# Kernel tuning notes

Hardware: AMD Instinct MI355X
Metric: run time of the kernel (lower is better)

## Reference

```python
import jax, jax.numpy as jnp
import numpy as np

B, N_STATES, STATE_SIZE = 32768, 16, 32
ENC, HID, OUT = 64, 128, 8


def setup_inputs() -> dict:
    key = jax.random.key(0)
    ks = jax.random.split(key, 8)
    states = jax.random.normal(ks[0], (B, N_STATES, STATE_SIZE), dtype=jnp.float32)
    # validity flags: first element of each per-field state. agent state (index 0)
    # always valid; neighbor states valid with prob 0.7 (contiguity enforced in reference
    # via cumprod, matching the original while-loop semantics).
    flags = (jax.random.uniform(ks[1], (B, N_STATES)) < 0.7).astype(jnp.float32)
    flags = flags.at[:, 0].set(1.0)
    states = states.at[:, :, 0].set(flags)
    obs_flat = states.reshape(B, N_STATES * STATE_SIZE)
    s = 0.05
    return {
        "obs_flat": obs_flat,
        "W_enc": jax.random.normal(ks[2], (STATE_SIZE, ENC), dtype=jnp.float32) * s,
        "b_enc": jnp.zeros((ENC,), dtype=jnp.float32),
        "W_f": jax.random.normal(ks[3], (2 * ENC, HID), dtype=jnp.float32) * s,
        "b_f": jnp.zeros((HID,), dtype=jnp.float32),
        "W_dec": jax.random.normal(ks[4], (HID, OUT), dtype=jnp.float32) * s,
        "b_dec": jnp.zeros((OUT,), dtype=jnp.float32),
    }


def reference(obs_flat, W_enc, b_enc, W_f, b_f, W_dec, b_dec):
    Bsz = obs_flat.shape[0]
    states = obs_flat.reshape(Bsz, N_STATES, STATE_SIZE)          # [B,N,S]
    flags = states[:, :, 0]                                        # [B,N]
    # original: while-loop stops at first invalid state -> contiguous-prefix validity
    neigh_valid = jnp.cumprod((flags[:, 1:] == 1.0).astype(jnp.float32), axis=1)  # [B,N-1]
    enc = jax.nn.relu(jnp.einsum('bns,se->bne', states, W_enc) + b_enc)            # [B,N,E]
    agent_enc = enc[:, 0]                                          # [B,E]
    neigh_enc = enc[:, 1:]                                         # [B,N-1,E]
    cnt = jnp.sum(neigh_valid, axis=1)                             # [B]
    # mean aggregation over valid neighbors; zero vector if none (original aggregates [zeros])
    agg = jnp.einsum('bne,bn->be', neigh_enc, neigh_valid) / jnp.maximum(cnt, 1.0)[:, None]
    f_in = jnp.concatenate([agent_enc, agg], axis=-1)              # [B,2E]
    hidden = jax.nn.relu(f_in @ W_f + b_f)                         # [B,H]
    logits = hidden @ W_dec + b_dec                                # [B,O]
    return logits
```

## Files before the change

kernel.cpp:

```cpp
#include <hip/hip_runtime.h>
#include <stdint.h>

#define NB    32768
#define NS    16
#define SS    32
#define ENCD  64
#define HIDD  128
#define OUTD  8
#define BT    32
#define THREADS 256

typedef short bf16x8 __attribute__((ext_vector_type(8)));
typedef float f32x4  __attribute__((ext_vector_type(4)));

#define MFMA(a, b, c) __builtin_amdgcn_mfma_f32_16x16x32_bf16((a), (b), (c), 0, 0, 0)

__device__ __forceinline__ short bf16_bits(float x) {
  union { float f; uint32_t u; } v; v.f = x;
  uint32_t u = v.u;
  uint32_t r = (u + 0x7FFFu + ((u >> 16) & 1u)) >> 16;
  return (short)r;
}
__device__ __forceinline__ float bf16_to_f(short h) {
  union { uint32_t u; float f; } v;
  v.u = ((uint32_t)(uint16_t)h) << 16;
  return v.f;
}
__device__ __forceinline__ void split8(const float* f, bf16x8& hi, bf16x8& lo) {
#pragma unroll
  for (int j = 0; j < 8; ++j) {
    short h = bf16_bits(f[j]);
    hi[j] = h;
    lo[j] = bf16_bits(f[j] - bf16_to_f(h));
  }
}

__global__ __launch_bounds__(THREADS)
void gnn_fused(const float* __restrict__ obs,
               const float* __restrict__ W_enc,
               const float* __restrict__ b_enc,
               const float* __restrict__ W_f,
               const float* __restrict__ b_f,
               const float* __restrict__ W_dec,
               const float* __restrict__ b_dec,
               float* __restrict__ out)
{
  __shared__ __align__(16) float f_in[BT][132];
  __shared__ __align__(16) float hidn[BT][132];

  const int tid  = threadIdx.x;
  const int w    = tid >> 6;
  const int l    = tid & 63;
  const int m15  = l & 15;
  const int quad = l >> 4;
  const int b0   = blockIdx.x * BT;

  bf16x8 we_hi[4], we_lo[4];
  float  benc[4];
#pragma unroll
  for (int nt = 0; nt < 4; ++nt) {
    float f[8];
#pragma unroll
    for (int j = 0; j < 8; ++j)
      f[j] = W_enc[(size_t)(quad * 8 + j) * ENCD + nt * 16 + m15];
    split8(f, we_hi[nt], we_lo[nt]);
    benc[nt] = b_enc[nt * 16 + m15];
  }

  const float* bp = obs + (size_t)(b0 + w * 8) * (NS * SS) + m15 * SS + quad * 8;
  float4 c0 = ((const float4*)bp)[0];
  float4 c1 = ((const float4*)bp)[1];
#pragma unroll
  for (int i = 0; i < 8; ++i) {
    float4 n0, n1;
    if (i < 7) {
      const float* np = bp + (size_t)(i + 1) * (NS * SS);
      n0 = ((const float4*)np)[0];
      n1 = ((const float4*)np)[1];
    } else { n0 = c0; n1 = c1; }

    float f[8] = {c0.x, c0.y, c0.z, c0.w, c1.x, c1.y, c1.z, c1.w};

    unsigned long long bal = __ballot((l < 16) && (f[0] == 1.0f));
    int run = __builtin_ctzll(~(bal >> 1));
    float inv = 1.0f / fmaxf((float)run, 1.0f);

    bf16x8 ahi, alo;
    split8(f, ahi, alo);

    const int bi = w * 8 + i;
#pragma unroll
    for (int nt = 0; nt < 4; ++nt) {
      f32x4 acc = {0.f, 0.f, 0.f, 0.f};
      acc = MFMA(ahi, we_hi[nt], acc);
      acc = MFMA(alo, we_hi[nt], acc);
      acc = MFMA(ahi, we_lo[nt], acc);
      float s = 0.f, e0 = 0.f;
#pragma unroll
      for (int r = 0; r < 4; ++r) {
        int n = quad * 4 + r;
        float v = fmaxf(acc[r] + benc[nt], 0.f);
        if (n == 0) e0 = v;
        if (n >= 1 && n <= run) s += v;
      }
      s += __shfl_xor(s, 16, 64);
      s += __shfl_xor(s, 32, 64);
      if (quad == 0) {
        f_in[bi][nt * 16 + m15]      = e0;
        f_in[bi][64 + nt * 16 + m15] = s * inv;
      }
    }
    c0 = n0; c1 = n1;
  }
  __syncthreads();

  {
    const int mt = w >> 1;
    const int hb = (w & 1) * 4;

    bf16x8 fa_hi[4], fa_lo[4];
#pragma unroll
    for (int ks = 0; ks < 4; ++ks) {
      const float4* p = (const float4*)&f_in[mt * 16 + m15][ks * 32 + quad * 8];
      float4 a = p[0], b = p[1];
      float f[8] = {a.x, a.y, a.z, a.w, b.x, b.y, b.z, b.w};
      split8(f, fa_hi[ks], fa_lo[ks]);
    }

#pragma unroll
    for (int t = 0; t < 4; ++t) {
      const int h0 = (hb + t) * 16 + m15;
      f32x4 acc = {0.f, 0.f, 0.f, 0.f};
#pragma unroll
      for (int ks = 0; ks < 4; ++ks) {
        float f[8];
#pragma unroll
        for (int j = 0; j < 8; ++j)
          f[j] = W_f[(size_t)(ks * 32 + quad * 8 + j) * HIDD + h0];
        bf16x8 bhi, blo;
        split8(f, bhi, blo);
        acc = MFMA(fa_hi[ks], bhi, acc);
        acc = MFMA(fa_lo[ks], bhi, acc);
        acc = MFMA(fa_hi[ks], blo, acc);
      }
      const float bfv = b_f[h0];
#pragma unroll
      for (int r = 0; r < 4; ++r)
        hidn[mt * 16 + quad * 4 + r][h0] = fmaxf(acc[r] + bfv, 0.f);
    }
  }
  __syncthreads();

  if (w < 2) {
    bf16x8 ga_hi[4], ga_lo[4];
#pragma unroll
    for (int ks = 0; ks < 4; ++ks) {
      const float4* p = (const float4*)&hidn[w * 16 + m15][ks * 32 + quad * 8];
      float4 a = p[0], b = p[1];
      float f[8] = {a.x, a.y, a.z, a.w, b.x, b.y, b.z, b.w};
      split8(f, ga_hi[ks], ga_lo[ks]);
    }
    f32x4 acc = {0.f, 0.f, 0.f, 0.f};
#pragma unroll
    for (int ks = 0; ks < 4; ++ks) {
      float f[8];
#pragma unroll
      for (int j = 0; j < 8; ++j) {
        int k = ks * 32 + quad * 8 + j;
        f[j] = (m15 < OUTD) ? W_dec[(size_t)k * OUTD + m15] : 0.f;
      }
      bf16x8 bhi, blo;
      split8(f, bhi, blo);
      acc = MFMA(ga_hi[ks], bhi, acc);
      acc = MFMA(ga_lo[ks], bhi, acc);
      acc = MFMA(ga_hi[ks], blo, acc);
    }
    if (m15 < OUTD) {
      const float bd = b_dec[m15];
#pragma unroll
      for (int r = 0; r < 4; ++r) {
        const int m = w * 16 + quad * 4 + r;
        out[(size_t)(b0 + m) * OUTD + m15] = acc[r] + bd;
      }
    }
  }
}

extern "C" void kernel_launch(void* const* d_in, const int* in_sizes, int n_in,
                              void* d_out, int out_size, void* d_ws, size_t ws_size,
                              hipStream_t stream) {
  (void)in_sizes; (void)n_in; (void)d_ws; (void)ws_size; (void)out_size;
  const float* obs   = (const float*)d_in[0];
  const float* W_enc = (const float*)d_in[1];
  const float* b_enc = (const float*)d_in[2];
  const float* W_f   = (const float*)d_in[3];
  const float* b_f   = (const float*)d_in[4];
  const float* W_dec = (const float*)d_in[5];
  const float* b_dec = (const float*)d_in[6];
  float* out = (float*)d_out;

  dim3 grid(NB / BT);
  dim3 block(THREADS);
  gnn_fused<<<grid, block, 0, stream>>>(obs, W_enc, b_enc, W_f, b_f, W_dec, b_dec, out);
}
```

Baseline: 121.5 us.

## Switch split-precision MFMA from bf16 to fp16 and halve batch tile per block

```diff
diff --git a/kernel.cpp b/kernel.cpp
--- a/kernel.cpp
+++ b/kernel.cpp
@@ -7,35 +7,28 @@
 #define ENCD  64
 #define HIDD  128
 #define OUTD  8
-#define BT    32
+#define BT    16
 #define THREADS 256
 
-typedef short bf16x8 __attribute__((ext_vector_type(8)));
-typedef float f32x4  __attribute__((ext_vector_type(4)));
+typedef _Float16 half8  __attribute__((ext_vector_type(8)));
+typedef __fp16   fp16x2 __attribute__((ext_vector_type(2)));
+typedef float    f32x4  __attribute__((ext_vector_type(4)));
 
-#define MFMA(a, b, c) __builtin_amdgcn_mfma_f32_16x16x32_bf16((a), (b), (c), 0, 0, 0)
+#define MFMA(a, b, c) __builtin_amdgcn_mfma_f32_16x16x32_f16((a), (b), (c), 0, 0, 0)
 
-__device__ __forceinline__ short bf16_bits(float x) {
-  union { float f; uint32_t u; } v; v.f = x;
-  uint32_t u = v.u;
-  uint32_t r = (u + 0x7FFFu + ((u >> 16) & 1u)) >> 16;
-  return (short)r;
-}
-__device__ __forceinline__ float bf16_to_f(short h) {
-  union { uint32_t u; float f; } v;
-  v.u = ((uint32_t)(uint16_t)h) << 16;
-  return v.f;
-}
-__device__ __forceinline__ void split8(const float* f, bf16x8& hi, bf16x8& lo) {
+__device__ __forceinline__ void split8(const float* f, half8& hi, half8& lo) {
 #pragma unroll
-  for (int j = 0; j < 8; ++j) {
-    short h = bf16_bits(f[j]);
-    hi[j] = h;
-    lo[j] = bf16_bits(f[j] - bf16_to_f(h));
+  for (int j = 0; j < 8; j += 2) {
+    fp16x2 h  = __builtin_amdgcn_cvt_pkrtz(f[j], f[j + 1]);
+    float  r0 = f[j]     - (float)h[0];
+    float  r1 = f[j + 1] - (float)h[1];
+    fp16x2 l2 = __builtin_amdgcn_cvt_pkrtz(r0, r1);
+    hi[j] = (_Float16)(float)h[0];  hi[j + 1] = (_Float16)(float)h[1];
+    lo[j] = (_Float16)(float)l2[0]; lo[j + 1] = (_Float16)(float)l2[1];
   }
 }
 
-__global__ __launch_bounds__(THREADS)
+__global__ __launch_bounds__(THREADS, 6)
 void gnn_fused(const float* __restrict__ obs,
                const float* __restrict__ W_enc,
                const float* __restrict__ b_enc,
@@ -55,8 +48,8 @@
   const int quad = l >> 4;
   const int b0   = blockIdx.x * BT;
 
-  bf16x8 we_hi[4], we_lo[4];
-  float  benc[4];
+  half8 we_hi[4], we_lo[4];
+  float benc[4];
 #pragma unroll
   for (int nt = 0; nt < 4; ++nt) {
     float f[8];
@@ -67,13 +60,13 @@
     benc[nt] = b_enc[nt * 16 + m15];
   }
 
-  const float* bp = obs + (size_t)(b0 + w * 8) * (NS * SS) + m15 * SS + quad * 8;
+  const float* bp = obs + (size_t)(b0 + w * 4) * (NS * SS) + m15 * SS + quad * 8;
   float4 c0 = ((const float4*)bp)[0];
   float4 c1 = ((const float4*)bp)[1];
 #pragma unroll
-  for (int i = 0; i < 8; ++i) {
+  for (int i = 0; i < 4; ++i) {
     float4 n0, n1;
-    if (i < 7) {
+    if (i < 3) {
       const float* np = bp + (size_t)(i + 1) * (NS * SS);
       n0 = ((const float4*)np)[0];
       n1 = ((const float4*)np)[1];
@@ -85,10 +78,10 @@
     int run = __builtin_ctzll(~(bal >> 1));
     float inv = 1.0f / fmaxf((float)run, 1.0f);
 
-    bf16x8 ahi, alo;
+    half8 ahi, alo;
     split8(f, ahi, alo);
 
-    const int bi = w * 8 + i;
+    const int bi = w * 4 + i;
 #pragma unroll
     for (int nt = 0; nt < 4; ++nt) {
       f32x4 acc = {0.f, 0.f, 0.f, 0.f};
@@ -115,21 +108,18 @@
   __syncthreads();
 
   {
-    const int mt = w >> 1;
-    const int hb = (w & 1) * 4;
-
-    bf16x8 fa_hi[4], fa_lo[4];
+    half8 fa_hi[4], fa_lo[4];
 #pragma unroll
     for (int ks = 0; ks < 4; ++ks) {
-      const float4* p = (const float4*)&f_in[mt * 16 + m15][ks * 32 + quad * 8];
+      const float4* p = (const float4*)&f_in[m15][ks * 32 + quad * 8];
       float4 a = p[0], b = p[1];
       float f[8] = {a.x, a.y, a.z, a.w, b.x, b.y, b.z, b.w};
       split8(f, fa_hi[ks], fa_lo[ks]);
     }
 
 #pragma unroll
-    for (int t = 0; t < 4; ++t) {
-      const int h0 = (hb + t) * 16 + m15;
+    for (int tt = 0; tt < 2; ++tt) {
+      const int h0 = (w * 2 + tt) * 16 + m15;
       f32x4 acc = {0.f, 0.f, 0.f, 0.f};
 #pragma unroll
       for (int ks = 0; ks < 4; ++ks) {
@@ -137,7 +127,7 @@
 #pragma unroll
         for (int j = 0; j < 8; ++j)
           f[j] = W_f[(size_t)(ks * 32 + quad * 8 + j) * HIDD + h0];
-        bf16x8 bhi, blo;
+        half8 bhi, blo;
         split8(f, bhi, blo);
         acc = MFMA(fa_hi[ks], bhi, acc);
         acc = MFMA(fa_lo[ks], bhi, acc);
@@ -146,16 +136,16 @@
       const float bfv = b_f[h0];
 #pragma unroll
       for (int r = 0; r < 4; ++r)
-        hidn[mt * 16 + quad * 4 + r][h0] = fmaxf(acc[r] + bfv, 0.f);
+        hidn[quad * 4 + r][h0] = fmaxf(acc[r] + bfv, 0.f);
     }
   }
   __syncthreads();
 
-  if (w < 2) {
-    bf16x8 ga_hi[4], ga_lo[4];
+  if (w == 0) {
+    half8 ga_hi[4], ga_lo[4];
 #pragma unroll
     for (int ks = 0; ks < 4; ++ks) {
-      const float4* p = (const float4*)&hidn[w * 16 + m15][ks * 32 + quad * 8];
+      const float4* p = (const float4*)&hidn[m15][ks * 32 + quad * 8];
       float4 a = p[0], b = p[1];
       float f[8] = {a.x, a.y, a.z, a.w, b.x, b.y, b.z, b.w};
       split8(f, ga_hi[ks], ga_lo[ks]);
@@ -169,7 +159,7 @@
         int k = ks * 32 + quad * 8 + j;
         f[j] = (m15 < OUTD) ? W_dec[(size_t)k * OUTD + m15] : 0.f;
       }
-      bf16x8 bhi, blo;
+      half8 bhi, blo;
       split8(f, bhi, blo);
       acc = MFMA(ga_hi[ks], bhi, acc);
       acc = MFMA(ga_lo[ks], bhi, acc);
@@ -179,7 +169,7 @@
       const float bd = b_dec[m15];
 #pragma unroll
       for (int r = 0; r < 4; ++r) {
-        const int m = w * 16 + quad * 4 + r;
+        const int m = quad * 4 + r;
         out[(size_t)(b0 + m) * OUTD + m15] = acc[r] + bd;
       }
     }
```

After: 111.3 us. 1.09x faster.
